# Optimization experiments

Measured on AMD Instinct MI355X. Metric: run time of the kernel, lower is better.

Reference implementation:

```python
import jax, jax.numpy as jnp
import numpy as np

B, N, DIN, D, HID, C, K = 16, 1024, 768, 512, 128, 20, 64
H = W = 32
EPS = 1e-5  # BatchNorm eps (inference mode with running stats)


def _conv(x, w, pad=0, dil=1):
    return jax.lax.conv_general_dilated(
        x, w, (1, 1), [(pad, pad), (pad, pad)],
        rhs_dilation=(dil, dil),
        dimension_numbers=('NCHW', 'OIHW', 'NCHW'))


def _bn(x, g, b, m, v):
    inv = jax.lax.rsqrt(v + EPS)
    return (x - m[None, :, None, None]) * (g * inv)[None, :, None, None] + b[None, :, None, None]


def _l2norm(x):
    n = jnp.sqrt(jnp.sum(x * x, axis=-1, keepdims=True))
    return x / jnp.maximum(n, 1e-12)  # matches F.normalize(eps=1e-12)


def setup_inputs():
    key = jax.random.key(0)
    ks = jax.random.split(key, 12)

    def conv_w(k, o, i, kh, kw):
        return jax.random.normal(k, (o, i, kh, kw), jnp.float32) / np.sqrt(i * kh * kw)

    def bn_p(k, c):
        k1, k2 = jax.random.split(k)
        return (jnp.ones(c, jnp.float32), jnp.zeros(c, jnp.float32),
                0.1 * jax.random.normal(k1, (c,), jnp.float32),
                jax.random.uniform(k2, (c,), jnp.float32, 0.5, 1.5))

    g0, b0, m0, v0 = bn_p(ks[3], D)
    gr, br, mr, vr = bn_p(ks[4], HID)
    gl, bl, ml, vl = bn_p(ks[5], HID)
    gg, bg, mg, vg = bn_p(ks[6], HID)
    gp, bp, mp, vp = bn_p(ks[7], D)
    return {
        'patch_feats': jax.random.normal(ks[0], (B, N, DIN), jnp.float32),
        'protos': _l2norm(jax.random.normal(ks[1], (C, K, D), jnp.float32)),  # hybrid protos, L2-normed as in __init__
        'w0': conv_w(ks[2], D, DIN, 1, 1), 'g0': g0, 'b0': b0, 'm0': m0, 'v0': v0,
        'wr': conv_w(ks[8], HID, D, 1, 1), 'gr': gr, 'br': br, 'mr': mr, 'vr': vr,
        'wl': conv_w(ks[9], HID, HID, 3, 3), 'gl': gl, 'bl': bl, 'ml': ml, 'vl': vl,
        'wg': conv_w(ks[10], HID, HID, 3, 3), 'gg': gg, 'bg': bg, 'mg': mg, 'vg': vg,
        'wp': conv_w(ks[11], D, 2 * HID, 1, 1), 'gp': gp, 'bp': bp, 'mp': mp, 'vp': vp,
        'wf': conv_w(jax.random.fold_in(key, 99), D, D, 1, 1),
        'bf': jnp.zeros(D, jnp.float32),
        'logit_scale': jnp.float32(10.0),
    }


def reference(patch_feats, protos, w0, g0, b0, m0, v0, wr, gr, br, mr, vr,
              wl, gl, bl, ml, vl, wg, gg, bg, mg, vg, wp, gp, bp, mp, vp,
              wf, bf, logit_scale):
    Bq, Nq, Din = patch_feats.shape
    x = patch_feats.transpose(0, 2, 1).reshape(Bq, Din, H, W)
    # adapter: 1x1 conv -> BN -> ReLU
    x = jax.nn.relu(_bn(_conv(x, w0), g0, b0, m0, v0))
    # ResidualContextBlock
    res = x
    o = jax.nn.relu(_bn(_conv(x, wr), gr, br, mr, vr))
    l = jax.nn.relu(_bn(_conv(o, wl, pad=1), gl, bl, ml, vl))
    g = jax.nn.relu(_bn(_conv(o, wg, pad=2, dil=2), gg, bg, mg, vg))
    o = _bn(_conv(jnp.concatenate([l, g], axis=1), wp), gp, bp, mp, vp)
    x = jax.nn.relu(o + res)
    # final 1x1 conv (with bias)
    x = _conv(x, wf) + bf[None, :, None, None]
    # back to [B, N, D], L2 normalize
    x = x.reshape(Bq, D, Nq).transpose(0, 2, 1)
    x = _l2norm(x)
    # per-class cosine sims + double max reduction (vectorized over classes)
    sims = jnp.einsum('bnd,ckd->bcnk', x, protos)  # [B,C,N,K]
    A = sims.max(axis=-1)                          # [B,C,N] patch->proto max
    act_maps = A.reshape(Bq, C, H, W)
    logits = A.max(axis=-1) * logit_scale          # [B,C]
    return logits, act_maps, x
```

## Files before the change

kernel.cpp:

```cpp
#include <hip/hip_runtime.h>
#include <math.h>

#define BN_EPS 1e-5f

typedef __attribute__((ext_vector_type(8))) short short8v;
typedef __attribute__((ext_vector_type(8))) unsigned short ushort8v;
typedef __attribute__((ext_vector_type(4))) float f32x4;

__device__ __forceinline__ unsigned short f2b(float f) {
    unsigned int u = __float_as_uint(f);
    return (unsigned short)((u + 0x7FFFu + ((u >> 16) & 1u)) >> 16);
}
__device__ __forceinline__ float b2f(unsigned short h) {
    return __uint_as_float(((unsigned int)h) << 16);
}

typedef __attribute__((address_space(1))) const unsigned int gas_uint;
typedef __attribute__((address_space(3))) unsigned int las_uint;
__device__ __forceinline__ void gload16(const void* g, void* l) {
    __builtin_amdgcn_global_load_lds((gas_uint*)g, (las_uint*)l, 16, 0, 0);
}

#define VMCNT4() asm volatile("s_waitcnt vmcnt(4)" ::: "memory")
#define VMCNT6() asm volatile("s_waitcnt vmcnt(6)" ::: "memory")
#define VMCNT0() asm volatile("s_waitcnt vmcnt(0)" ::: "memory")
#define LGKM0()  asm volatile("s_waitcnt lgkmcnt(0)" ::: "memory")
#define SBAR()   __builtin_amdgcn_s_barrier()
#define SCHED0() __builtin_amdgcn_sched_barrier(0)

__global__ __launch_bounds__(256) void f2b_kernel(
    const float* __restrict__ in, unsigned short* __restrict__ out, int n8)
{
    int i = blockIdx.x * 256 + threadIdx.x;
    if (i >= n8) return;
    const float4* p = (const float4*)(in + (size_t)i * 8);
    float4 a = p[0], b = p[1];
    ushort8v r;
    r[0] = f2b(a.x); r[1] = f2b(a.y); r[2] = f2b(a.z); r[3] = f2b(a.w);
    r[4] = f2b(b.x); r[5] = f2b(b.y); r[6] = f2b(b.z); r[7] = f2b(b.w);
    *(ushort8v*)(out + (size_t)i * 8) = r;
}

__global__ __launch_bounds__(256) void f2b_multi(
    const float* __restrict__ w0, const float* __restrict__ wr,
    const float* __restrict__ wp, const float* __restrict__ wf,
    const float* __restrict__ prot,
    unsigned short* __restrict__ w0o, unsigned short* __restrict__ wro,
    unsigned short* __restrict__ wpo, unsigned short* __restrict__ wfo,
    unsigned short* __restrict__ proto)
{
    int i = blockIdx.x * 256 + threadIdx.x;
    const float* src; unsigned short* dst; int off;
    if      (i <  49152) { src = w0;   dst = w0o;   off = i; }
    else if (i <  57344) { src = wr;   dst = wro;   off = i - 49152; }
    else if (i <  73728) { src = wp;   dst = wpo;   off = i - 57344; }
    else if (i < 106496) { src = wf;   dst = wfo;   off = i - 73728; }
    else if (i < 188416) { src = prot; dst = proto; off = i - 106496; }
    else return;
    const float4* p = (const float4*)(src + (size_t)off * 8);
    float4 a = p[0], b = p[1];
    ushort8v r;
    r[0] = f2b(a.x); r[1] = f2b(a.y); r[2] = f2b(a.z); r[3] = f2b(a.w);
    r[4] = f2b(b.x); r[5] = f2b(b.y); r[6] = f2b(b.z); r[7] = f2b(b.w);
    *(ushort8v*)(dst + (size_t)off * 8) = r;
}

__global__ __launch_bounds__(256) void convw_kernel(
    const float* __restrict__ wl, const float* __restrict__ wg,
    unsigned short* __restrict__ out)
{
    int i = blockIdx.x * 256 + threadIdx.x;
    if (i >= 294912) return;
    int br = i >= 147456;
    int j  = i - br * 147456;
    int tap = j >> 14, oc = (j >> 7) & 127, ic = j & 127;
    const float* src = br ? wg : wl;
    out[i] = f2b(src[((oc << 7) + ic) * 9 + tap]);
}

__global__ __launch_bounds__(256) void zero_kernel(unsigned short* __restrict__ p, int n8)
{
    int i = blockIdx.x * 256 + threadIdx.x;
    if (i >= n8) return;
    ushort8v z;
#pragma unroll
    for (int k = 0; k < 8; ++k) z[k] = 0;
    *(ushort8v*)(p + (size_t)i * 8) = z;
}

template <int EPI>
__global__ __launch_bounds__(256, 3) void mfma_gemm(
    const unsigned short* __restrict__ A, int lda,
    const unsigned short* __restrict__ Wt, int ldw,
    void* __restrict__ outp, int ldc, int Kdim,
    const float* __restrict__ bng, const float* __restrict__ bnb,
    const float* __restrict__ bnm, const float* __restrict__ bnv,
    const unsigned short* __restrict__ res, int ldres,
    const float* __restrict__ bias)
{
    __shared__ short8v Asta[2][512];
    __shared__ short8v Bsta[2][512];
    const int t  = threadIdx.x;
    const int l  = t & 63, wv = t >> 6;
    const int wm = wv >> 1, wn = wv & 1;
    const int m0 = blockIdx.x << 7, n0 = blockIdx.y << 7;

    const int r0  = t & 127;
    const int kb0 = t >> 7;

    const unsigned short* Ap = A  + (size_t)(m0 + r0) * lda + kb0 * 8;
    const unsigned short* Bp = Wt + (size_t)(n0 + r0) * ldw + kb0 * 8;

    f32x4 acc[4][4];
#pragma unroll
    for (int mf = 0; mf < 4; ++mf)
#pragma unroll
        for (int nf = 0; nf < 4; ++nf)
#pragma unroll
            for (int j = 0; j < 4; ++j) acc[mf][nf][j] = 0.f;

    const int arow = wm * 64 + (l & 15);
    const int brow = wn * 64 + (l & 15);
    const int kq   = l >> 4;

    const int nK = Kdim >> 5;

#define STAGE_G(buf, k0)                                     \
    do {                                                     \
        gload16(Ap + (k0),      &Asta[buf][wv * 64]);        \
        gload16(Ap + (k0) + 16, &Asta[buf][wv * 64 + 256]);  \
        gload16(Bp + (k0),      &Bsta[buf][wv * 64]);        \
        gload16(Bp + (k0) + 16, &Bsta[buf][wv * 64 + 256]);  \
    } while (0)

    STAGE_G(0, 0);
    int cur = 0;
    for (int ks = 0; ks < nK; ++ks) {
        if (ks + 1 < nK) { STAGE_G(cur ^ 1, (ks + 1) << 5); VMCNT4(); }
        else             { VMCNT0(); }
        SBAR();
        short8v af[4], bfv[4];
#pragma unroll
        for (int mf = 0; mf < 4; ++mf) af[mf]  = Asta[cur][kq * 128 + arow + mf * 16];
#pragma unroll
        for (int nf = 0; nf < 4; ++nf) bfv[nf] = Bsta[cur][kq * 128 + brow + nf * 16];
#pragma unroll
        for (int mf = 0; mf < 4; ++mf)
#pragma unroll
            for (int nf = 0; nf < 4; ++nf)
                acc[mf][nf] = __builtin_amdgcn_mfma_f32_16x16x32_bf16(
                    af[mf], bfv[nf], acc[mf][nf], 0, 0, 0);
        LGKM0(); SCHED0();
        SBAR();
        cur ^= 1;
    }
#undef STAGE_G

    float s[4], sh[4];
    int cols[4];
#pragma unroll
    for (int nf = 0; nf < 4; ++nf) {
        int col = n0 + wn * 64 + nf * 16 + (l & 15);
        cols[nf] = col;
        if (EPI == 2) { s[nf] = 1.f; sh[nf] = bias[col]; }
        else {
            float sc = bng[col] * rsqrtf(bnv[col] + BN_EPS);
            s[nf]  = sc;
            sh[nf] = bnb[col] - bnm[col] * sc;
        }
    }
#pragma unroll
    for (int mf = 0; mf < 4; ++mf) {
#pragma unroll
        for (int j = 0; j < 4; ++j) {
            int row = m0 + wm * 64 + mf * 16 + kq * 4 + j;
#pragma unroll
            for (int nf = 0; nf < 4; ++nf) {
                float v = acc[mf][nf][j] * s[nf] + sh[nf];
                if (EPI == 1) v += b2f(res[(size_t)row * ldres + cols[nf]]);
                if (EPI != 2) v = fmaxf(v, 0.f);
                if (EPI == 2) {
                    ((float*)outp)[(size_t)row * ldc + cols[nf]] = v;
                } else if (EPI == 3) {
                    int b = row >> 10, h = (row >> 5) & 31, ww = row & 31;
                    size_t pidx = ((size_t)(b * 36 + h + 2) * 36 + (ww + 2)) * 128 + cols[nf];
                    ((unsigned short*)outp)[pidx] = f2b(v);
                } else {
                    ((unsigned short*)outp)[(size_t)row * ldc + cols[nf]] = f2b(v);
                }
            }
        }
    }
}

__global__ __launch_bounds__(256, 3) void conv_mfma(
    const unsigned short* __restrict__ opad,
    const unsigned short* __restrict__ wt_all,
    const float* __restrict__ g1, const float* __restrict__ b1,
    const float* __restrict__ m1, const float* __restrict__ v1,
    const float* __restrict__ g2, const float* __restrict__ b2,
    const float* __restrict__ m2, const float* __restrict__ v2,
    unsigned short* __restrict__ lg)
{
    __shared__ short8v Asta[2][512];
    __shared__ short8v Bsta[2][1024];
    const int t = threadIdx.x;
    const int l = t & 63, wv = t >> 6;
    const int wm = wv >> 1, wn = wv & 1;
    const int m0 = blockIdx.x << 6;
    const int br = blockIdx.y;
    const int dil = 1 + br;
    const unsigned short* wtb = wt_all + (size_t)br * 147456;

    const int r0 = t & 63;
    const int m  = m0 + r0;
    const int bb = m >> 10, h = (m >> 5) & 31, wc = m & 31;
    const ptrdiff_t pbase = ((ptrdiff_t)(bb * 36 + h + 2) * 36 + (wc + 2)) * 128;
    const unsigned short* ApT = opad + pbase + (t >> 6) * 8;
    const unsigned short* BpT = wtb + (size_t)(t & 127) * 128 + (t >> 7) * 8;

    f32x4 acc[2][4];
#pragma unroll
    for (int mf = 0; mf < 2; ++mf)
#pragma unroll
        for (int nf = 0; nf < 4; ++nf)
#pragma unroll
            for (int j = 0; j < 4; ++j) acc[mf][nf][j] = 0.f;

    const int arow = wm * 32 + (l & 15);
    const int bcol = wn * 64 + (l & 15);
    const int kq   = l >> 4;

#define STAGE_C(buf, s)                                                        \
    do {                                                                       \
        int tap_ = (s) >> 1, hh_ = ((s) & 1) * 64;                             \
        int dh_ = tap_ / 3 - 1, dw_ = tap_ % 3 - 1;                            \
        const unsigned short* Ap_ = ApT + (ptrdiff_t)((dh_ * 36 + dw_) * dil) * 128 + hh_; \
        const unsigned short* Bp_ = BpT + (size_t)tap_ * 16384 + hh_;          \
        gload16(Ap_,      &Asta[buf][wv * 64]);                                \
        gload16(Ap_ + 32, &Asta[buf][wv * 64 + 256]);                          \
        gload16(Bp_,      &Bsta[buf][wv * 64]);                                \
        gload16(Bp_ + 16, &Bsta[buf][wv * 64 + 256]);                          \
        gload16(Bp_ + 32, &Bsta[buf][wv * 64 + 512]);                          \
        gload16(Bp_ + 48, &Bsta[buf][wv * 64 + 768]);                          \
    } while (0)

    STAGE_C(0, 0);
    int cur = 0;
    for (int s = 0; s < 18; ++s) {
        if (s + 1 < 18) { STAGE_C(cur ^ 1, s + 1); VMCNT6(); }
        else            { VMCNT0(); }
        SBAR();
        short8v af[2][2], bfv[2][4];
#pragma unroll
        for (int kk = 0; kk < 2; ++kk) {
            int kb = kk * 4 + kq;
            af[kk][0] = Asta[cur][kb * 64 + arow];
            af[kk][1] = Asta[cur][kb * 64 + arow + 16];
#pragma unroll
            for (int nf = 0; nf < 4; ++nf)
                bfv[kk][nf] = Bsta[cur][kb * 128 + bcol + nf * 16];
        }
#pragma unroll
        for (int kk = 0; kk < 2; ++kk)
#pragma unroll
            for (int mf = 0; mf < 2; ++mf)
#pragma unroll
                for (int nf = 0; nf < 4; ++nf)
                    acc[mf][nf] = __builtin_amdgcn_mfma_f32_16x16x32_bf16(
                        af[kk][mf], bfv[kk][nf], acc[mf][nf], 0, 0, 0);
        LGKM0(); SCHED0();
        SBAR();
        cur ^= 1;
    }
#undef STAGE_C

    const float* gg = br ? g2 : g1;
    const float* gb = br ? b2 : b1;
    const float* gm = br ? m2 : m1;
    const float* gv = br ? v2 : v1;
    float s4[4], sh[4];
    int cols[4];
#pragma unroll
    for (int nf = 0; nf < 4; ++nf) {
        int col = bcol + nf * 16;
        cols[nf] = col;
        float sc = gg[col] * rsqrtf(gv[col] + BN_EPS);
        s4[nf] = sc;
        sh[nf] = gb[col] - gm[col] * sc;
    }
#pragma unroll
    for (int mf = 0; mf < 2; ++mf) {
#pragma unroll
        for (int j = 0; j < 4; ++j) {
            int row = m0 + wm * 32 + mf * 16 + kq * 4 + j;
#pragma unroll
            for (int nf = 0; nf < 4; ++nf) {
                float v = fmaxf(acc[mf][nf][j] * s4[nf] + sh[nf], 0.f);
                lg[(size_t)row * 256 + br * 128 + cols[nf]] = f2b(v);
            }
        }
    }
}

__global__ __launch_bounds__(256) void l2norm_rows(
    float* __restrict__ x, unsigned short* __restrict__ xn)
{
    const int t    = threadIdx.x;
    const int wv   = t >> 6, lane = t & 63;
    const int row  = (blockIdx.x << 2) + wv;
    float* p = x + (size_t)row * 512 + (lane << 3);
    float4 a = *(float4*)p;
    float4 b = *(float4*)(p + 4);
    float ss = a.x * a.x + a.y * a.y + a.z * a.z + a.w * a.w +
               b.x * b.x + b.y * b.y + b.z * b.z + b.w * b.w;
#pragma unroll
    for (int off = 32; off >= 1; off >>= 1) ss += __shfl_xor(ss, off);
    float sc = 1.f / fmaxf(sqrtf(ss), 1e-12f);
    a.x *= sc; a.y *= sc; a.z *= sc; a.w *= sc;
    b.x *= sc; b.y *= sc; b.z *= sc; b.w *= sc;
    *(float4*)p       = a;
    *(float4*)(p + 4) = b;
    ushort8v r;
    r[0] = f2b(a.x); r[1] = f2b(a.y); r[2] = f2b(a.z); r[3] = f2b(a.w);
    r[4] = f2b(b.x); r[5] = f2b(b.y); r[6] = f2b(b.z); r[7] = f2b(b.w);
    *(ushort8v*)(xn + (size_t)row * 512 + (lane << 3)) = r;
}

__global__ __launch_bounds__(256, 3) void sims_mfma(
    const unsigned short* __restrict__ xn,
    const unsigned short* __restrict__ protos,
    float* __restrict__ act)
{
    __shared__ short8v Asta[2][512];
    __shared__ short8v Bsta[2][512];
    const int t = threadIdx.x;
    const int l = t & 63, wv = t >> 6;
    const int wm = wv >> 1, wn = wv & 1;
    const int m0 = blockIdx.x << 7;

    const int r0  = t & 127, kb0 = t >> 7;
    const unsigned short* Ap = xn + (size_t)(m0 + r0) * 512 + kb0 * 8;
    const unsigned short* Bp = protos + ((size_t)blockIdx.y * 128 + r0) * 512 + kb0 * 8;

    f32x4 acc[4][4];
#pragma unroll
    for (int mf = 0; mf < 4; ++mf)
#pragma unroll
        for (int nf = 0; nf < 4; ++nf)
#pragma unroll
            for (int j = 0; j < 4; ++j) acc[mf][nf][j] = 0.f;

    const int arow = wm * 64 + (l & 15);
    const int brow = wn * 64 + (l & 15);
    const int kq   = l >> 4;

#define STAGE_S(buf, k0)                                     \
    do {                                                     \
        gload16(Ap + (k0),      &Asta[buf][wv * 64]);        \
        gload16(Ap + (k0) + 16, &Asta[buf][wv * 64 + 256]);  \
        gload16(Bp + (k0),      &Bsta[buf][wv * 64]);        \
        gload16(Bp + (k0) + 16, &Bsta[buf][wv * 64 + 256]);  \
    } while (0)

    STAGE_S(0, 0);
    int cur = 0;
    for (int ks = 0; ks < 16; ++ks) {
        if (ks + 1 < 16) { STAGE_S(cur ^ 1, (ks + 1) << 5); VMCNT4(); }
        else             { VMCNT0(); }
        SBAR();
        short8v af[4], bfv[4];
#pragma unroll
        for (int mf = 0; mf < 4; ++mf) af[mf]  = Asta[cur][kq * 128 + arow + mf * 16];
#pragma unroll
        for (int nf = 0; nf < 4; ++nf) bfv[nf] = Bsta[cur][kq * 128 + brow + nf * 16];
#pragma unroll
        for (int mf = 0; mf < 4; ++mf)
#pragma unroll
            for (int nf = 0; nf < 4; ++nf)
                acc[mf][nf] = __builtin_amdgcn_mfma_f32_16x16x32_bf16(
                    af[mf], bfv[nf], acc[mf][nf], 0, 0, 0);
        LGKM0(); SCHED0();
        SBAR();
        cur ^= 1;
    }
#undef STAGE_S

    const int c = (blockIdx.y << 1) + wn;
#pragma unroll
    for (int mf = 0; mf < 4; ++mf) {
        float vj[4];
#pragma unroll
        for (int j = 0; j < 4; ++j) {
            float v = fmaxf(fmaxf(acc[mf][0][j], acc[mf][1][j]),
                            fmaxf(acc[mf][2][j], acc[mf][3][j]));
            v = fmaxf(v, __shfl_xor(v, 1));
            v = fmaxf(v, __shfl_xor(v, 2));
            v = fmaxf(v, __shfl_xor(v, 4));
            v = fmaxf(v, __shfl_xor(v, 8));
            vj[j] = v;
        }
        if ((l & 15) == 0) {
            int rowb = m0 + wm * 64 + mf * 16 + kq * 4;
#pragma unroll
            for (int j = 0; j < 4; ++j) {
                int row = rowb + j;
                int bb = row >> 10, n = row & 1023;
                act[(((size_t)(bb * 20 + c)) << 10) + n] = vj[j];
            }
        }
    }
}

__global__ __launch_bounds__(256) void logits_max(
    const float* __restrict__ act, const float* __restrict__ lsc,
    float* __restrict__ logits)
{
    const int bc = blockIdx.x;
    const int t  = threadIdx.x;
    float4 v = *(const float4*)(act + ((size_t)bc << 10) + (t << 2));
    float mx = fmaxf(fmaxf(v.x, v.y), fmaxf(v.z, v.w));
#pragma unroll
    for (int off = 32; off >= 1; off >>= 1) mx = fmaxf(mx, __shfl_xor(mx, off));
    __shared__ float wmred[4];
    if ((t & 63) == 0) wmred[t >> 6] = mx;
    __syncthreads();
    if (t == 0) {
        float m2 = fmaxf(fmaxf(wmred[0], wmred[1]), fmaxf(wmred[2], wmred[3]));
        logits[bc] = m2 * lsc[0];
    }
}

extern "C" void kernel_launch(void* const* d_in, const int* in_sizes, int n_in,
                              void* d_out, int out_size, void* d_ws, size_t ws_size,
                              hipStream_t stream)
{
    const float* pf   = (const float*)d_in[0];
    const float* prot = (const float*)d_in[1];
    const float* w0   = (const float*)d_in[2];
    const float* g0   = (const float*)d_in[3];
    const float* b0   = (const float*)d_in[4];
    const float* m0v  = (const float*)d_in[5];
    const float* v0   = (const float*)d_in[6];
    const float* wr   = (const float*)d_in[7];
    const float* gr   = (const float*)d_in[8];
    const float* br   = (const float*)d_in[9];
    const float* mr   = (const float*)d_in[10];
    const float* vr   = (const float*)d_in[11];
    const float* wl   = (const float*)d_in[12];
    const float* gl   = (const float*)d_in[13];
    const float* bl   = (const float*)d_in[14];
    const float* ml   = (const float*)d_in[15];
    const float* vl   = (const float*)d_in[16];
    const float* wg   = (const float*)d_in[17];
    const float* gG   = (const float*)d_in[18];
    const float* bG   = (const float*)d_in[19];
    const float* mG   = (const float*)d_in[20];
    const float* vG   = (const float*)d_in[21];
    const float* wp   = (const float*)d_in[22];
    const float* gp   = (const float*)d_in[23];
    const float* bp   = (const float*)d_in[24];
    const float* mp   = (const float*)d_in[25];
    const float* vp   = (const float*)d_in[26];
    const float* wf   = (const float*)d_in[27];
    const float* bf_  = (const float*)d_in[28];
    const float* lsc  = (const float*)d_in[29];

    char* ws = (char*)d_ws;
    unsigned short* pf_bf    = (unsigned short*)(ws);
    unsigned short* w0_bf    = (unsigned short*)(ws + 25165824);
    unsigned short* wr_bf    = (unsigned short*)(ws + 25952256);
    unsigned short* wt_bf    = (unsigned short*)(ws + 26083328);
    unsigned short* wp_bf    = (unsigned short*)(ws + 26673152);
    unsigned short* wf_bf    = (unsigned short*)(ws + 26935296);
    unsigned short* prot_bf  = (unsigned short*)(ws + 27459584);
    unsigned short* x1_bf    = (unsigned short*)(ws + 28770304);
    unsigned short* opad     = (unsigned short*)(ws + 45547520);
    unsigned short* lg_bf    = (unsigned short*)(ws + 50855936);
    unsigned short* x2_bf    = (unsigned short*)(ws + 59244544);
    unsigned short* xn_bf    = (unsigned short*)(ws + 76021760);

    float* out    = (float*)d_out;
    float* logits = out;
    float* act    = out + 320;
    float* xo     = out + 328000;

    f2b_kernel<<<6144, 256, 0, stream>>>(pf, pf_bf, 1572864);
    f2b_multi<<<736, 256, 0, stream>>>(w0, wr, wp, wf, prot,
                                       w0_bf, wr_bf, wp_bf, wf_bf, prot_bf);
    convw_kernel<<<1152, 256, 0, stream>>>(wl, wg, wt_bf);
    zero_kernel<<<1296, 256, 0, stream>>>(opad, 331776);

    mfma_gemm<0><<<dim3(128, 4), 256, 0, stream>>>(
        pf_bf, 768, w0_bf, 768, x1_bf, 512, 768,
        g0, b0, m0v, v0, nullptr, 0, nullptr);

    mfma_gemm<3><<<dim3(128, 1), 256, 0, stream>>>(
        x1_bf, 512, wr_bf, 512, opad, 0, 512,
        gr, br, mr, vr, nullptr, 0, nullptr);

    conv_mfma<<<dim3(256, 2), 256, 0, stream>>>(
        opad, wt_bf, gl, bl, ml, vl, gG, bG, mG, vG, lg_bf);

    mfma_gemm<1><<<dim3(128, 4), 256, 0, stream>>>(
        lg_bf, 256, wp_bf, 256, x2_bf, 512, 256,
        gp, bp, mp, vp, x1_bf, 512, nullptr);

    mfma_gemm<2><<<dim3(128, 4), 256, 0, stream>>>(
        x2_bf, 512, wf_bf, 512, xo, 512, 512,
        nullptr, nullptr, nullptr, nullptr, nullptr, 0, bf_);

    l2norm_rows<<<4096, 256, 0, stream>>>(xo, xn_bf);

    sims_mfma<<<dim3(128, 10), 256, 0, stream>>>(xn_bf, prot_bf, act);

    logits_max<<<320, 256, 0, stream>>>(act, lsc, logits);
}
```

Before: 199.9 us.

## Fuse prep kernels and restructure sims to keep bf16 features resident in LDS

Merges the four preprocessing launches (feature cast, weight casts, conv weight transpose, pad zeroing) into one kernel. The l2norm no longer writes a bf16 copy. The similarity kernel now loads a 64-row fp32 tile, converts it to bf16 into LDS once, and streams all 20 class prototype sets through double-buffered LDS, reducing the max per class. This trades a 1280-block grid with full re-reads for 256 blocks with large LDS use, which may lower occupancy and parallelism.

```diff
diff --git a/kernel.cpp b/kernel.cpp
--- a/kernel.cpp
+++ b/kernel.cpp
@@ -21,71 +21,60 @@
     __builtin_amdgcn_global_load_lds((gas_uint*)g, (las_uint*)l, 16, 0, 0);
 }
 
-#define VMCNT4() asm volatile("s_waitcnt vmcnt(4)" ::: "memory")
-#define VMCNT6() asm volatile("s_waitcnt vmcnt(6)" ::: "memory")
-#define VMCNT0() asm volatile("s_waitcnt vmcnt(0)" ::: "memory")
-#define LGKM0()  asm volatile("s_waitcnt lgkmcnt(0)" ::: "memory")
-#define SBAR()   __builtin_amdgcn_s_barrier()
-#define SCHED0() __builtin_amdgcn_sched_barrier(0)
-
-__global__ __launch_bounds__(256) void f2b_kernel(
-    const float* __restrict__ in, unsigned short* __restrict__ out, int n8)
+#define VMCNT4()  asm volatile("s_waitcnt vmcnt(4)"  ::: "memory")
+#define VMCNT6()  asm volatile("s_waitcnt vmcnt(6)"  ::: "memory")
+#define VMCNT0()  asm volatile("s_waitcnt vmcnt(0)"  ::: "memory")
+#define LGKM0()   asm volatile("s_waitcnt lgkmcnt(0)" ::: "memory")
+#define SBAR()    __builtin_amdgcn_s_barrier()
+#define SCHED0()  __builtin_amdgcn_sched_barrier(0)
+
+__global__ __launch_bounds__(256) void prep_all(
+    const float* __restrict__ pf,  const float* __restrict__ w0,
+    const float* __restrict__ wr,  const float* __restrict__ wp,
+    const float* __restrict__ wf,  const float* __restrict__ prot,
+    const float* __restrict__ wl,  const float* __restrict__ wg,
+    unsigned short* __restrict__ pf_o, unsigned short* __restrict__ w0_o,
+    unsigned short* __restrict__ wr_o, unsigned short* __restrict__ wp_o,
+    unsigned short* __restrict__ wf_o, unsigned short* __restrict__ prot_o,
+    unsigned short* __restrict__ wt_o, unsigned short* __restrict__ opad)
 {
     int i = blockIdx.x * 256 + threadIdx.x;
-    if (i >= n8) return;
-    const float4* p = (const float4*)(in + (size_t)i * 8);
-    float4 a = p[0], b = p[1];
-    ushort8v r;
-    r[0] = f2b(a.x); r[1] = f2b(a.y); r[2] = f2b(a.z); r[3] = f2b(a.w);
-    r[4] = f2b(b.x); r[5] = f2b(b.y); r[6] = f2b(b.z); r[7] = f2b(b.w);
-    *(ushort8v*)(out + (size_t)i * 8) = r;
-}
-
-__global__ __launch_bounds__(256) void f2b_multi(
-    const float* __restrict__ w0, const float* __restrict__ wr,
-    const float* __restrict__ wp, const float* __restrict__ wf,
-    const float* __restrict__ prot,
-    unsigned short* __restrict__ w0o, unsigned short* __restrict__ wro,
-    unsigned short* __restrict__ wpo, unsigned short* __restrict__ wfo,
-    unsigned short* __restrict__ proto)
-{
-    int i = blockIdx.x * 256 + threadIdx.x;
+    if (i >= 2129920) return;
+    if (i >= 1798144) {
+        ushort8v z;
+#pragma unroll
+        for (int k = 0; k < 8; ++k) z[k] = 0;
+        *(ushort8v*)(opad + (size_t)(i - 1798144) * 8) = z;
+        return;
+    }
+    if (i >= 1761280) {
+        int e0 = (i - 1761280) * 8;
+        ushort8v u;
+#pragma unroll
+        for (int q = 0; q < 8; ++q) {
+            int e = e0 + q;
+            int br = e >= 147456;
+            int j  = e - br * 147456;
+            int tap = j >> 14, oc = (j >> 7) & 127, ic = j & 127;
+            const float* src = br ? wg : wl;
+            u[q] = f2b(src[((oc << 7) + ic) * 9 + tap]);
+        }
+        *(ushort8v*)(wt_o + (size_t)e0) = u;
+        return;
+    }
     const float* src; unsigned short* dst; int off;
-    if      (i <  49152) { src = w0;   dst = w0o;   off = i; }
-    else if (i <  57344) { src = wr;   dst = wro;   off = i - 49152; }
-    else if (i <  73728) { src = wp;   dst = wpo;   off = i - 57344; }
-    else if (i < 106496) { src = wf;   dst = wfo;   off = i - 73728; }
-    else if (i < 188416) { src = prot; dst = proto; off = i - 106496; }
-    else return;
+    if      (i <  1572864) { src = pf;   dst = pf_o;   off = i; }
+    else if (i <  1622016) { src = w0;   dst = w0_o;   off = i - 1572864; }
+    else if (i <  1630208) { src = wr;   dst = wr_o;   off = i - 1622016; }
+    else if (i <  1646592) { src = wp;   dst = wp_o;   off = i - 1630208; }
+    else if (i <  1679360) { src = wf;   dst = wf_o;   off = i - 1646592; }
+    else                   { src = prot; dst = prot_o; off = i - 1679360; }
     const float4* p = (const float4*)(src + (size_t)off * 8);
     float4 a = p[0], b = p[1];
     ushort8v r;
     r[0] = f2b(a.x); r[1] = f2b(a.y); r[2] = f2b(a.z); r[3] = f2b(a.w);
     r[4] = f2b(b.x); r[5] = f2b(b.y); r[6] = f2b(b.z); r[7] = f2b(b.w);
     *(ushort8v*)(dst + (size_t)off * 8) = r;
-}
-
-__global__ __launch_bounds__(256) void convw_kernel(
-    const float* __restrict__ wl, const float* __restrict__ wg,
-    unsigned short* __restrict__ out)
-{
-    int i = blockIdx.x * 256 + threadIdx.x;
-    if (i >= 294912) return;
-    int br = i >= 147456;
-    int j  = i - br * 147456;
-    int tap = j >> 14, oc = (j >> 7) & 127, ic = j & 127;
-    const float* src = br ? wg : wl;
-    out[i] = f2b(src[((oc << 7) + ic) * 9 + tap]);
-}
-
-__global__ __launch_bounds__(256) void zero_kernel(unsigned short* __restrict__ p, int n8)
-{
-    int i = blockIdx.x * 256 + threadIdx.x;
-    if (i >= n8) return;
-    ushort8v z;
-#pragma unroll
-    for (int k = 0; k < 8; ++k) z[k] = 0;
-    *(ushort8v*)(p + (size_t)i * 8) = z;
 }
 
 template <int EPI>
@@ -122,8 +111,7 @@
     const int arow = wm * 64 + (l & 15);
     const int brow = wn * 64 + (l & 15);
     const int kq   = l >> 4;
-
-    const int nK = Kdim >> 5;
+    const int nK   = Kdim >> 5;
 
 #define STAGE_G(buf, k0)                                     \
     do {                                                     \
@@ -303,8 +291,7 @@
     }
 }
 
-__global__ __launch_bounds__(256) void l2norm_rows(
-    float* __restrict__ x, unsigned short* __restrict__ xn)
+__global__ __launch_bounds__(256) void l2norm_rows(float* __restrict__ x)
 {
     const int t    = threadIdx.x;
     const int wv   = t >> 6, lane = t & 63;
@@ -321,95 +308,123 @@
     b.x *= sc; b.y *= sc; b.z *= sc; b.w *= sc;
     *(float4*)p       = a;
     *(float4*)(p + 4) = b;
-    ushort8v r;
-    r[0] = f2b(a.x); r[1] = f2b(a.y); r[2] = f2b(a.z); r[3] = f2b(a.w);
-    r[4] = f2b(b.x); r[5] = f2b(b.y); r[6] = f2b(b.z); r[7] = f2b(b.w);
-    *(ushort8v*)(xn + (size_t)row * 512 + (lane << 3)) = r;
-}
-
-__global__ __launch_bounds__(256, 3) void sims_mfma(
-    const unsigned short* __restrict__ xn,
+}
+
+__global__ __launch_bounds__(256) void sims_fused(
+    const float* __restrict__ xo,
     const unsigned short* __restrict__ protos,
     float* __restrict__ act)
 {
-    __shared__ short8v Asta[2][512];
-    __shared__ short8v Bsta[2][512];
+    __shared__ short8v Alds[4096];
+    __shared__ short8v Blds[2][1024];
     const int t = threadIdx.x;
     const int l = t & 63, wv = t >> 6;
     const int wm = wv >> 1, wn = wv & 1;
-    const int m0 = blockIdx.x << 7;
-
-    const int r0  = t & 127, kb0 = t >> 7;
-    const unsigned short* Ap = xn + (size_t)(m0 + r0) * 512 + kb0 * 8;
-    const unsigned short* Bp = protos + ((size_t)blockIdx.y * 128 + r0) * 512 + kb0 * 8;
-
-    f32x4 acc[4][4];
-#pragma unroll
-    for (int mf = 0; mf < 4; ++mf)
+    const int m0 = blockIdx.x << 6;
+
+    {
+        const int r = t >> 2, ksb = (t & 3) << 7;
+        const float* src = xo + (size_t)(m0 + r) * 512 + ksb;
+#pragma unroll
+        for (int j = 0; j < 16; ++j) {
+            float4 a = *(const float4*)(src + j * 8);
+            float4 b = *(const float4*)(src + j * 8 + 4);
+            ushort8v u;
+            u[0] = f2b(a.x); u[1] = f2b(a.y); u[2] = f2b(a.z); u[3] = f2b(a.w);
+            u[4] = f2b(b.x); u[5] = f2b(b.y); u[6] = f2b(b.z); u[7] = f2b(b.w);
+            int kb = (ksb >> 3) + j;
+            *(ushort8v*)&Alds[kb * 64 + r] = u;
+        }
+    }
+
+    const unsigned short* Bp = protos + (size_t)(t & 127) * 512 + (t >> 7) * 8;
+#define STAGE_B(buf, S)                                                         \
+    do {                                                                        \
+        const unsigned short* q_ = Bp + (size_t)((S) >> 3) * 65536 + (((S) & 7) << 6); \
+        _Pragma("unroll")                                                       \
+        for (int i_ = 0; i_ < 4; ++i_)                                          \
+            gload16(q_ + 16 * i_, &Blds[buf][wv * 64 + 256 * i_]);              \
+    } while (0)
+
+    f32x4 acc[2][4];
+#pragma unroll
+    for (int mf = 0; mf < 2; ++mf)
 #pragma unroll
         for (int nf = 0; nf < 4; ++nf)
 #pragma unroll
             for (int j = 0; j < 4; ++j) acc[mf][nf][j] = 0.f;
 
-    const int arow = wm * 64 + (l & 15);
+    const int arow = wm * 32 + (l & 15);
     const int brow = wn * 64 + (l & 15);
     const int kq   = l >> 4;
 
-#define STAGE_S(buf, k0)                                     \
-    do {                                                     \
-        gload16(Ap + (k0),      &Asta[buf][wv * 64]);        \
-        gload16(Ap + (k0) + 16, &Asta[buf][wv * 64 + 256]);  \
-        gload16(Bp + (k0),      &Bsta[buf][wv * 64]);        \
-        gload16(Bp + (k0) + 16, &Bsta[buf][wv * 64 + 256]);  \
-    } while (0)
-
-    STAGE_S(0, 0);
+    STAGE_B(0, 0);
+    VMCNT0(); LGKM0();
+    SBAR();
     int cur = 0;
-    for (int ks = 0; ks < 16; ++ks) {
-        if (ks + 1 < 16) { STAGE_S(cur ^ 1, (ks + 1) << 5); VMCNT4(); }
-        else             { VMCNT0(); }
+    for (int S = 0; S < 80; ++S) {
+        if (S + 1 < 80) { STAGE_B(cur ^ 1, S + 1); VMCNT4(); }
+        else            { VMCNT0(); }
         SBAR();
-        short8v af[4], bfv[4];
-#pragma unroll
-        for (int mf = 0; mf < 4; ++mf) af[mf]  = Asta[cur][kq * 128 + arow + mf * 16];
-#pragma unroll
-        for (int nf = 0; nf < 4; ++nf) bfv[nf] = Bsta[cur][kq * 128 + brow + nf * 16];
-#pragma unroll
-        for (int mf = 0; mf < 4; ++mf)
+        const int ks = S & 7;
+        short8v af[2][2], bfv[2][4];
+#pragma unroll
+        for (int kk = 0; kk < 2; ++kk) {
+            int kb  = ks * 8 + kq + 4 * kk;
+            int kb8 = kq + 4 * kk;
+            af[kk][0] = Alds[kb * 64 + arow];
+            af[kk][1] = Alds[kb * 64 + arow + 16];
 #pragma unroll
             for (int nf = 0; nf < 4; ++nf)
-                acc[mf][nf] = __builtin_amdgcn_mfma_f32_16x16x32_bf16(
-                    af[mf], bfv[nf], acc[mf][nf], 0, 0, 0);
+                bfv[kk][nf] = Blds[cur][kb8 * 128 + brow + nf * 16];
+        }
+        LGKM0(); SCHED0();
+        __builtin_amdgcn_s_setprio(1);
+#pragma unroll
+        for (int kk = 0; kk < 2; ++kk)
+#pragma unroll
+            for (int mf = 0; mf < 2; ++mf)
+#pragma unroll
+                for (int nf = 0; nf < 4; ++nf)
+                    acc[mf][nf] = __builtin_amdgcn_mfma_f32_16x16x32_bf16(
+                        af[kk][mf], bfv[kk][nf], acc[mf][nf], 0, 0, 0);
+        __builtin_amdgcn_s_setprio(0);
         LGKM0(); SCHED0();
         SBAR();
+        if (ks == 7) {
+            const int cp = S >> 3;
+            const int c  = cp * 2 + wn;
+#pragma unroll
+            for (int mf = 0; mf < 2; ++mf) {
+                float vj[4];
+#pragma unroll
+                for (int j = 0; j < 4; ++j) {
+                    float v = fmaxf(fmaxf(acc[mf][0][j], acc[mf][1][j]),
+                                    fmaxf(acc[mf][2][j], acc[mf][3][j]));
+                    v = fmaxf(v, __shfl_xor(v, 1));
+                    v = fmaxf(v, __shfl_xor(v, 2));
+                    v = fmaxf(v, __shfl_xor(v, 4));
+                    v = fmaxf(v, __shfl_xor(v, 8));
+                    vj[j] = v;
+                }
+                if ((l & 15) == 0) {
+                    int rowb = m0 + wm * 32 + mf * 16 + kq * 4;
+#pragma unroll
+                    for (int j = 0; j < 4; ++j) {
+                        int row = rowb + j;
+                        int bb = row >> 10, n = row & 1023;
+                        act[(((size_t)(bb * 20 + c)) << 10) + n] = vj[j];
+                    }
+                }
+#pragma unroll
+                for (int nf = 0; nf < 4; ++nf)
+#pragma unroll
+                    for (int j = 0; j < 4; ++j) acc[mf][nf][j] = 0.f;
+            }
+        }
         cur ^= 1;
     }
-#undef STAGE_S
-
-    const int c = (blockIdx.y << 1) + wn;
-#pragma unroll
-    for (int mf = 0; mf < 4; ++mf) {
-        float vj[4];
-#pragma unroll
-        for (int j = 0; j < 4; ++j) {
-            float v = fmaxf(fmaxf(acc[mf][0][j], acc[mf][1][j]),
-                            fmaxf(acc[mf][2][j], acc[mf][3][j]));
-            v = fmaxf(v, __shfl_xor(v, 1));
-            v = fmaxf(v, __shfl_xor(v, 2));
-            v = fmaxf(v, __shfl_xor(v, 4));
-            v = fmaxf(v, __shfl_xor(v, 8));
-            vj[j] = v;
-        }
-        if ((l & 15) == 0) {
-            int rowb = m0 + wm * 64 + mf * 16 + kq * 4;
-#pragma unroll
-            for (int j = 0; j < 4; ++j) {
-                int row = rowb + j;
-                int bb = row >> 10, n = row & 1023;
-                act[(((size_t)(bb * 20 + c)) << 10) + n] = vj[j];
-            }
-        }
-    }
+#undef STAGE_B
 }
 
 __global__ __launch_bounds__(256) void logits_max(
@@ -478,18 +493,15 @@
     unsigned short* opad     = (unsigned short*)(ws + 45547520);
     unsigned short* lg_bf    = (unsigned short*)(ws + 50855936);
     unsigned short* x2_bf    = (unsigned short*)(ws + 59244544);
-    unsigned short* xn_bf    = (unsigned short*)(ws + 76021760);
 
     float* out    = (float*)d_out;
     float* logits = out;
     float* act    = out + 320;
     float* xo     = out + 328000;
 
-    f2b_kernel<<<6144, 256, 0, stream>>>(pf, pf_bf, 1572864);
-    f2b_multi<<<736, 256, 0, stream>>>(w0, wr, wp, wf, prot,
-                                       w0_bf, wr_bf, wp_bf, wf_bf, prot_bf);
-    convw_kernel<<<1152, 256, 0, stream>>>(wl, wg, wt_bf);
-    zero_kernel<<<1296, 256, 0, stream>>>(opad, 331776);
+    prep_all<<<8320, 256, 0, stream>>>(
+        pf, w0, wr, wp, wf, prot, wl, wg,
+        pf_bf, w0_bf, wr_bf, wp_bf, wf_bf, prot_bf, wt_bf, opad);
 
     mfma_gemm<0><<<dim3(128, 4), 256, 0, stream>>>(
         pf_bf, 768, w0_bf, 768, x1_bf, 512, 768,
@@ -510,9 +522,9 @@
         x2_bf, 512, wf_bf, 512, xo, 512, 512,
         nullptr, nullptr, nullptr, nullptr, nullptr, 0, bf_);
 
-    l2norm_rows<<<4096, 256, 0, stream>>>(xo, xn_bf);
-
-    sims_mfma<<<dim3(128, 10), 256, 0, stream>>>(xn_bf, prot_bf, act);
+    l2norm_rows<<<4096, 256, 0, stream>>>(xo);
+
+    sims_fused<<<256, 256, 0, stream>>>(xo, prot_bf, act);
 
     logits_max<<<320, 256, 0, stream>>>(act, lsc, logits);
 }
```

Result: slower. 250.0 us (+25.1%).
